# Performance work log

Hardware: AMD Instinct MI355X
Metric: run time of the kernel (lower is better)

The kernel has to match this reference:

```python
import jax, jax.numpy as jnp
import numpy as np
from math import floor, ceil

B, CIN, COUT, H, W, K = 1, 8, 8, 1024, 1024, 31


def setup_inputs() -> dict:
    key = jax.random.key(0)
    k1, k2, k3 = jax.random.split(key, 3)
    signal = jax.random.normal(k1, (B, CIN, H, W), dtype=jnp.float32)
    weight = jax.random.normal(k2, (COUT, CIN, K, K), dtype=jnp.float32)
    bias = jax.random.normal(k3, (COUT,), dtype=jnp.float32)
    return {"signal": signal, "weight": weight, "bias": bias}


def reference(signal, weight, bias):
    # FFT-based cross-correlation with padding='same', stride=1, dilation=1, groups=1
    kh, kw = weight.shape[2], weight.shape[3]
    ph, pw = (kh - 1) / 2, (kw - 1) / 2
    # 'same' padding: floor/ceil split per side (torch f.pad order: last dim first)
    s = jnp.pad(signal, ((0, 0), (0, 0), (floor(ph), ceil(ph)), (floor(pw), ceil(pw))))
    Hs, Ws = s.shape[2], s.shape[3]  # padded signal size used for the output crop
    # torch pads last dim to even length for rfft efficiency
    if s.shape[3] % 2 != 0:
        s = jnp.pad(s, ((0, 0), (0, 0), (0, 0), (0, 1)))
    # zero-pad kernel up to the (even-padded) signal size
    kpad = jnpp = jnp.pad(weight, ((0, 0), (0, 0), (0, s.shape[2] - kh), (0, s.shape[3] - kw)))
    sig_fr = jnp.fft.rfftn(s, axes=(2, 3))            # [B, Cin, Hs, Wf]
    ker_fr = jnp.conj(jnp.fft.rfftn(kpad, axes=(2, 3)))  # conj -> cross-correlation
    out_fr = sig_fr * ker_fr                           # broadcast: [Cout, Cin, Hs, Wf] (B==1)
    out = jnp.fft.irfftn(out_fr, axes=(2, 3))          # [Cout, Cin, Hs, Ws_even]
    out = out[:, :, : Hs - kh + 1, : Ws - kw + 1]      # valid crop (stride 1)
    # bias.view(1, -1, 1, 1): broadcasts over dim1 (== Cin == Cout here)
    return out + bias.reshape(1, -1, 1, 1)
```

## Files before the change

### kernel.cpp

```cpp
#include <hip/hip_runtime.h>


typedef _Float16 f16x8 __attribute__((ext_vector_type(8)));
typedef float    f32x4 __attribute__((ext_vector_type(4)));

#define TY   16
#define TXB  64
#define SR   46
#define SDW  48
#define SROW 52

__device__ unsigned int g_wpk[8 * 8 * 31 * 16];

__global__ void wpack(const float* __restrict__ wgt) {
  int t = blockIdx.x * 256 + threadIdx.x;
  if (t >= 8 * 8 * 31) return;
  const int i = t % 31;
  const int o = (t / 31) & 7;
  const int c = t / 248;
  const float* src = wgt + (((o * 8) + c) * 31 + i) * 31;
  unsigned int* dst = g_wpk + (((c * 8) + o) * 31 + i) * 16;
  #pragma unroll
  for (int d = 0; d < 16; ++d) {
    float w0 = src[2 * d];
    float w1 = (2 * d + 1 < 31) ? src[2 * d + 1] : 0.f;
    union { _Float16 h[2]; unsigned int u; } p;
    p.h[0] = (_Float16)w0; p.h[1] = (_Float16)w1;
    dst[d] = p.u;
  }
}

__global__ __launch_bounds__(256, 4)
void conv_mfma(const float* __restrict__ sig,
               const float* __restrict__ bias,
               float* __restrict__ out) {
  __shared__ __align__(16) unsigned int ldss[SR * SROW];
  __shared__ __align__(16) unsigned int ldsw[8 * 31 * 16];

  const int tid = threadIdx.x;
  const int c  = blockIdx.z;
  const int x0 = blockIdx.x * TXB;
  const int y0 = blockIdx.y * TY;

  const float* sc = sig + c * (1024 * 1024);
  for (int f = tid; f < SR * SDW; f += 256) {
    const int r = f / SDW;
    const int d = f - r * SDW;
    const int gy = y0 + r - 15;
    const int gx = x0 + 2 * d - 15;
    float s0 = 0.f, s1 = 0.f;
    if ((unsigned)gy < 1024u) {
      const float* srcr = sc + gy * 1024;
      if ((unsigned)gx < 1024u)       s0 = srcr[gx];
      if ((unsigned)(gx + 1) < 1024u) s1 = srcr[gx + 1];
    }
    union { _Float16 h[2]; unsigned int u; } p;
    p.h[0] = (_Float16)s0; p.h[1] = (_Float16)s1;
    ldss[r * SROW + d] = p.u;
  }
  for (int f = tid; f < 8 * 31 * 16; f += 256) ldsw[f] = g_wpk[c * (8 * 31 * 16) + f];
  __syncthreads();

  const int lane = tid & 63;
  const int wv   = tid >> 6;
  const int n    = lane & 15;
  const int kg   = lane >> 4;
  const int xw   = wv * 16;

  f32x4 acc[16];
  #pragma unroll
  for (int xi = 0; xi < 16; ++xi) acc[xi] = (f32x4){0.f, 0.f, 0.f, 0.f};

  const unsigned int* wbase = &ldsw[(lane & 7) * 31 * 16 + kg * 4];

  for (int i = 0; i < 31; ++i) {
    union { uint4 v; f16x8 h; } au;
    au.v = *(const uint4*)(wbase + i * 16);
    const f16x8 af = au.h;

    const unsigned int* rowp = &ldss[(n + i) * SROW + 4 * kg + 8 * wv];
    const uint4 R0 = *(const uint4*)(rowp);
    const uint4 R1 = *(const uint4*)(rowp + 4);
    const uint4 R2 = *(const uint4*)(rowp + 8);
    const unsigned int W[12] = {R0.x, R0.y, R0.z, R0.w,
                                R1.x, R1.y, R1.z, R1.w,
                                R2.x, R2.y, R2.z, R2.w};
    unsigned int A_[11];
    #pragma unroll
    for (int d = 0; d < 11; ++d)
      A_[d] = __builtin_amdgcn_alignbit(W[d + 1], W[d], 16);

    #pragma unroll
    for (int xg = 0; xg < 4; ++xg) {
      const int d0 = 2 * xg;
      union { unsigned int u[4]; f16x8 h; } b0, b1, b2, b3;
      b0.u[0] = W[d0];      b0.u[1] = W[d0 + 1];  b0.u[2] = W[d0 + 2];  b0.u[3] = W[d0 + 3];
      b1.u[0] = A_[d0];     b1.u[1] = A_[d0 + 1]; b1.u[2] = A_[d0 + 2]; b1.u[3] = A_[d0 + 3];
      b2.u[0] = W[d0 + 1];  b2.u[1] = W[d0 + 2];  b2.u[2] = W[d0 + 3];  b2.u[3] = W[d0 + 4];
      b3.u[0] = A_[d0 + 1]; b3.u[1] = A_[d0 + 2]; b3.u[2] = A_[d0 + 3]; b3.u[3] = A_[d0 + 4];
      acc[4*xg+0] = __builtin_amdgcn_mfma_f32_16x16x32_f16(af, b0.h, acc[4*xg+0], 0, 0, 0);
      acc[4*xg+1] = __builtin_amdgcn_mfma_f32_16x16x32_f16(af, b1.h, acc[4*xg+1], 0, 0, 0);
      acc[4*xg+2] = __builtin_amdgcn_mfma_f32_16x16x32_f16(af, b2.h, acc[4*xg+2], 0, 0, 0);
      acc[4*xg+3] = __builtin_amdgcn_mfma_f32_16x16x32_f16(af, b3.h, acc[4*xg+3], 0, 0, 0);
    }
  }

  if (lane < 32) {
    const float bv = bias[c];
    const int y  = y0 + n;
    const int hi = lane >> 4;
    #pragma unroll
    for (int r = 0; r < 4; ++r) {
      const int o = hi * 4 + r;
      float* op = out + (((size_t)(o * 8 + c) * 1024 + y) * 1024 + x0 + xw);
      #pragma unroll
      for (int g = 0; g < 4; ++g) {
        float4 v;
        v.x = acc[4*g+0][r] + bv;
        v.y = acc[4*g+1][r] + bv;
        v.z = acc[4*g+2][r] + bv;
        v.w = acc[4*g+3][r] + bv;
        *(float4*)(op + 4*g) = v;
      }
    }
  }
}

extern "C" void kernel_launch(void* const* d_in, const int* in_sizes, int n_in,
                              void* d_out, int out_size, void* d_ws, size_t ws_size,
                              hipStream_t stream) {
  const float* sig  = (const float*)d_in[0];
  const float* wgt  = (const float*)d_in[1];
  const float* bias = (const float*)d_in[2];
  float* out = (float*)d_out;

  wpack<<<(8 * 8 * 31 + 255) / 256, 256, 0, stream>>>(wgt);
  dim3 grid(1024 / TXB, 1024 / TY, 8);
  conv_mfma<<<grid, 256, 0, stream>>>(sig, bias, out);
}
```

Before: 481.7 us.

## Fold odd-pixel shift into weights so MFMA M covers two output phases

The weight pack now builds a 16-row A matrix holding each output channel twice: unshifted for even x and shifted by one tap for odd x. Each MFMA therefore computes both even and odd pixels, which halves the MFMA count per row and removes the alignbit repacking. Weights are read straight from global memory with a one-step register prefetch instead of being staged through LDS. The epilogue uses cross-lane shuffles to interleave even and odd results so every lane writes contiguous float4s, at the cost of extra shuffles and selects.

```diff
diff --git a/kernel.cpp b/kernel.cpp
--- a/kernel.cpp
+++ b/kernel.cpp
@@ -10,32 +10,34 @@
 #define SDW  48
 #define SROW 52
 
-__device__ unsigned int g_wpk[8 * 8 * 31 * 16];
+__device__ unsigned int g_wA[8 * 31 * 256];
 
 __global__ void wpack(const float* __restrict__ wgt) {
   int t = blockIdx.x * 256 + threadIdx.x;
-  if (t >= 8 * 8 * 31) return;
-  const int i = t % 31;
-  const int o = (t / 31) & 7;
-  const int c = t / 248;
-  const float* src = wgt + (((o * 8) + c) * 31 + i) * 31;
-  unsigned int* dst = g_wpk + (((c * 8) + o) * 31 + i) * 16;
-  #pragma unroll
-  for (int d = 0; d < 16; ++d) {
-    float w0 = src[2 * d];
-    float w1 = (2 * d + 1 < 31) ? src[2 * d + 1] : 0.f;
-    union { _Float16 h[2]; unsigned int u; } p;
-    p.h[0] = (_Float16)w0; p.h[1] = (_Float16)w1;
-    dst[d] = p.u;
-  }
+  if (t >= 8 * 31 * 256) return;
+  const int d  = t & 3;
+  const int m  = (t >> 2) & 15;
+  const int kg = (t >> 6) & 3;
+  const int r  = t >> 8;
+  const int i  = r % 31;
+  const int c  = r / 31;
+  const int o  = m & 7;
+  const int s  = m >> 3;
+  const int k0 = kg * 8 + 2 * d;
+  const int j0 = k0 - s, j1 = k0 + 1 - s;
+  const float* wsrc = wgt + ((o * 8 + c) * 31 + i) * 31;
+  const float w0 = ((unsigned)j0 < 31u) ? wsrc[j0] : 0.f;
+  const float w1 = ((unsigned)j1 < 31u) ? wsrc[j1] : 0.f;
+  union { _Float16 h[2]; unsigned int u; } p;
+  p.h[0] = (_Float16)w0; p.h[1] = (_Float16)w1;
+  g_wA[t] = p.u;
 }
 
 __global__ __launch_bounds__(256, 4)
-void conv_mfma(const float* __restrict__ sig,
-               const float* __restrict__ bias,
-               float* __restrict__ out) {
+void conv_mfma2(const float* __restrict__ sig,
+                const float* __restrict__ bias,
+                float* __restrict__ out) {
   __shared__ __align__(16) unsigned int ldss[SR * SROW];
-  __shared__ __align__(16) unsigned int ldsw[8 * 31 * 16];
 
   const int tid = threadIdx.x;
   const int c  = blockIdx.z;
@@ -58,7 +60,6 @@
     p.h[0] = (_Float16)s0; p.h[1] = (_Float16)s1;
     ldss[r * SROW + d] = p.u;
   }
-  for (int f = tid; f < 8 * 31 * 16; f += 256) ldsw[f] = g_wpk[c * (8 * 31 * 16) + f];
   __syncthreads();
 
   const int lane = tid & 63;
@@ -67,62 +68,63 @@
   const int kg   = lane >> 4;
   const int xw   = wv * 16;
 
-  f32x4 acc[16];
+  f32x4 acc[8];
   #pragma unroll
-  for (int xi = 0; xi < 16; ++xi) acc[xi] = (f32x4){0.f, 0.f, 0.f, 0.f};
+  for (int xg = 0; xg < 8; ++xg) acc[xg] = (f32x4){0.f, 0.f, 0.f, 0.f};
 
-  const unsigned int* wbase = &ldsw[(lane & 7) * 31 * 16 + kg * 4];
+  const uint4* wq = (const uint4*)g_wA + c * (31 * 64) + lane;
+  uint4 wnext = wq[0];
 
   for (int i = 0; i < 31; ++i) {
     union { uint4 v; f16x8 h; } au;
-    au.v = *(const uint4*)(wbase + i * 16);
-    const f16x8 af = au.h;
+    au.v = wnext;
+    if (i < 30) wnext = wq[(i + 1) * 64];
 
-    const unsigned int* rowp = &ldss[(n + i) * SROW + 4 * kg + 8 * wv];
+    const unsigned int* rowp = &ldss[(n + i) * SROW + 8 * wv + 4 * kg];
     const uint4 R0 = *(const uint4*)(rowp);
     const uint4 R1 = *(const uint4*)(rowp + 4);
     const uint4 R2 = *(const uint4*)(rowp + 8);
     const unsigned int W[12] = {R0.x, R0.y, R0.z, R0.w,
                                 R1.x, R1.y, R1.z, R1.w,
                                 R2.x, R2.y, R2.z, R2.w};
-    unsigned int A_[11];
     #pragma unroll
-    for (int d = 0; d < 11; ++d)
-      A_[d] = __builtin_amdgcn_alignbit(W[d + 1], W[d], 16);
-
-    #pragma unroll
-    for (int xg = 0; xg < 4; ++xg) {
-      const int d0 = 2 * xg;
-      union { unsigned int u[4]; f16x8 h; } b0, b1, b2, b3;
-      b0.u[0] = W[d0];      b0.u[1] = W[d0 + 1];  b0.u[2] = W[d0 + 2];  b0.u[3] = W[d0 + 3];
-      b1.u[0] = A_[d0];     b1.u[1] = A_[d0 + 1]; b1.u[2] = A_[d0 + 2]; b1.u[3] = A_[d0 + 3];
-      b2.u[0] = W[d0 + 1];  b2.u[1] = W[d0 + 2];  b2.u[2] = W[d0 + 3];  b2.u[3] = W[d0 + 4];
-      b3.u[0] = A_[d0 + 1]; b3.u[1] = A_[d0 + 2]; b3.u[2] = A_[d0 + 3]; b3.u[3] = A_[d0 + 4];
-      acc[4*xg+0] = __builtin_amdgcn_mfma_f32_16x16x32_f16(af, b0.h, acc[4*xg+0], 0, 0, 0);
-      acc[4*xg+1] = __builtin_amdgcn_mfma_f32_16x16x32_f16(af, b1.h, acc[4*xg+1], 0, 0, 0);
-      acc[4*xg+2] = __builtin_amdgcn_mfma_f32_16x16x32_f16(af, b2.h, acc[4*xg+2], 0, 0, 0);
-      acc[4*xg+3] = __builtin_amdgcn_mfma_f32_16x16x32_f16(af, b3.h, acc[4*xg+3], 0, 0, 0);
+    for (int xg = 0; xg < 8; ++xg) {
+      union { unsigned int u[4]; f16x8 h; } b;
+      b.u[0] = W[xg]; b.u[1] = W[xg + 1]; b.u[2] = W[xg + 2]; b.u[3] = W[xg + 3];
+      acc[xg] = __builtin_amdgcn_mfma_f32_16x16x32_f16(au.h, b.h, acc[xg], 0, 0, 0);
     }
   }
 
-  if (lane < 32) {
-    const float bv = bias[c];
-    const int y  = y0 + n;
-    const int hi = lane >> 4;
+  const float bv  = bias[c];
+  const int  h    = kg >> 1;
+  const int  olo  = (kg & 1) * 4;
+  const int  y    = y0 + n;
+  const bool low  = (kg < 2);
+
+  #pragma unroll
+  for (int r = 0; r < 4; ++r) {
+    float av[8], pv[8];
     #pragma unroll
-    for (int r = 0; r < 4; ++r) {
-      const int o = hi * 4 + r;
-      float* op = out + (((size_t)(o * 8 + c) * 1024 + y) * 1024 + x0 + xw);
-      #pragma unroll
-      for (int g = 0; g < 4; ++g) {
-        float4 v;
-        v.x = acc[4*g+0][r] + bv;
-        v.y = acc[4*g+1][r] + bv;
-        v.z = acc[4*g+2][r] + bv;
-        v.w = acc[4*g+3][r] + bv;
-        *(float4*)(op + 4*g) = v;
-      }
+    for (int xg = 0; xg < 8; ++xg) {
+      av[xg] = acc[xg][r] + bv;
+      pv[xg] = __shfl_xor(av[xg], 32);
     }
+    const int o = olo + r;
+    float* op = out + (((size_t)(o * 8 + c) * 1024 + y) * 1024 + x0 + xw + 8 * h);
+    float4 v0, v1;
+    if (h == 0) {
+      v0.x = low ? av[0] : pv[0]; v0.y = low ? pv[0] : av[0];
+      v0.z = low ? av[1] : pv[1]; v0.w = low ? pv[1] : av[1];
+      v1.x = low ? av[2] : pv[2]; v1.y = low ? pv[2] : av[2];
+      v1.z = low ? av[3] : pv[3]; v1.w = low ? pv[3] : av[3];
+    } else {
+      v0.x = low ? av[4] : pv[4]; v0.y = low ? pv[4] : av[4];
+      v0.z = low ? av[5] : pv[5]; v0.w = low ? pv[5] : av[5];
+      v1.x = low ? av[6] : pv[6]; v1.y = low ? pv[6] : av[6];
+      v1.z = low ? av[7] : pv[7]; v1.w = low ? pv[7] : av[7];
+    }
+    *(float4*)(op)     = v0;
+    *(float4*)(op + 4) = v1;
   }
 }
 
@@ -134,7 +136,7 @@
   const float* bias = (const float*)d_in[2];
   float* out = (float*)d_out;
 
-  wpack<<<(8 * 8 * 31 + 255) / 256, 256, 0, stream>>>(wgt);
+  wpack<<<(8 * 31 * 256 + 255) / 256, 256, 0, stream>>>(wgt);
   dim3 grid(1024 / TXB, 1024 / TY, 8);
-  conv_mfma<<<grid, 256, 0, stream>>>(sig, bias, out);
+  conv_mfma2<<<grid, 256, 0, stream>>>(sig, bias, out);
 }
```

After: 410.0 us. -14.9%, faster.
